# Performance work log

Hardware: AMD Instinct MI355X
Metric: run time of the kernel (lower is better)

The kernel has to match this reference:

```python
import jax, jax.numpy as jnp
import numpy as np

H = 512

def setup_inputs() -> dict:
    key = jax.random.key(0)
    k1, k2, k3, k4 = jax.random.split(key, 4)
    B, S_dec, S_enc = 8, 2048, 2048
    encoder_output = jax.random.normal(k1, (B, S_enc, H), dtype=jnp.float32)
    decoder_output = jax.random.normal(k2, (B, S_dec, H), dtype=jnp.float32)
    # nn.Bilinear(H, H, 1): weight [1, H, H], bias [1]; init U(-1/sqrt(H), 1/sqrt(H))
    bound = 1.0 / np.sqrt(H)
    W = jax.random.uniform(k3, (1, H, H), dtype=jnp.float32, minval=-bound, maxval=bound)
    b = jax.random.uniform(k4, (1,), dtype=jnp.float32, minval=-bound, maxval=bound)
    return {"encoder_output": encoder_output, "decoder_output": decoder_output, "W": W, "b": b}

def reference(encoder_output, decoder_output, W, b):
    # Original: scores[b,d,e] = Bilinear(enc[b,e], dec[b,d]) = enc[b,e] @ W[0] @ dec[b,d] + bias
    # Computed as two GEMMs instead of expanding to [B, S_dec, S_enc, H].
    encW = jnp.einsum('beh,hg->beg', encoder_output, W[0])   # [B, S_enc, H]
    scores = jnp.einsum('beg,bdg->bde', encW, decoder_output) + b[0]  # [B, S_dec, S_enc]
    return scores
```

## Files before the change

kernel.cpp:

```cpp
#include <hip/hip_runtime.h>

typedef __attribute__((ext_vector_type(8))) short short8;
typedef __attribute__((ext_vector_type(4))) float f32x4;
typedef __attribute__((ext_vector_type(8))) unsigned short ushort8;

__device__ __forceinline__ unsigned short f2bf(float x) {
  union { float f; unsigned u; } v; v.f = x;
  unsigned r = v.u + 0x7fffu + ((v.u >> 16) & 1u);
  return (unsigned short)(r >> 16);
}

__global__ __launch_bounds__(256) void wt_kernel(
    const float* __restrict__ W, unsigned short* __restrict__ Wt) {
  __shared__ float s[64][65];
  int g0 = blockIdx.x * 64, h0 = blockIdx.y * 64;
  int tx = threadIdx.x & 63, ty = threadIdx.x >> 6;
#pragma unroll
  for (int rr = 0; rr < 16; ++rr) {
    int h = ty * 16 + rr;
    s[h][tx] = W[(long)(h0 + h) * 512 + g0 + tx];
  }
  __syncthreads();
#pragma unroll
  for (int rr = 0; rr < 16; ++rr) {
    int g = ty * 16 + rr;
    Wt[(long)(g0 + g) * 512 + h0 + tx] = f2bf(s[tx][g]);
  }
}

__global__ __launch_bounds__(256) void gemm1_plus_cvtdec(
    const float* __restrict__ enc, const unsigned short* __restrict__ Wt,
    unsigned short* __restrict__ encW,
    const float* __restrict__ dec, unsigned short* __restrict__ dec_bf) {
  if (blockIdx.x >= 512) {
    int i = (blockIdx.x - 512) * 256 + threadIdx.x;
    const float4* p = (const float4*)(dec + (long)i * 8);
    float4 a = p[0], b = p[1];
    ushort8 o;
    o[0] = f2bf(a.x); o[1] = f2bf(a.y); o[2] = f2bf(a.z); o[3] = f2bf(a.w);
    o[4] = f2bf(b.x); o[5] = f2bf(b.y); o[6] = f2bf(b.z); o[7] = f2bf(b.w);
    *(ushort8*)(dec_bf + (long)i * 8) = o;
    return;
  }

  constexpr int K = 512, N = 512, BK = 32;
  __shared__ __align__(16) short As[128 * BK];
  __shared__ __align__(16) short Bs[128 * BK];

  const int g = blockIdx.x;
  const int work = (g & 7) * 64 + (g >> 3);
  const int bxm = work >> 2, byn = work & 3;

  const int tid = threadIdx.x;
  const int wave = tid >> 6, lane = tid & 63;
  const int wm = wave >> 1, wn = wave & 1;
  const int r = lane & 15, q = lane >> 4;

  const float* Ab = enc + (long)bxm * 128 * K;
  const unsigned short* Bb = Wt + (long)byn * 128 * K;

  const int srow = tid >> 1, shalf = tid & 1;
  const float* arow = Ab + (long)srow * K + shalf * 16;

  f32x4 acc[4][4] = {};
  float4 av[4];
#pragma unroll
  for (int j = 0; j < 4; ++j) av[j] = ((const float4*)arow)[j];

  for (int kt = 0; kt < K; kt += BK) {
    ushort8 o0, o1;
    o0[0] = f2bf(av[0].x); o0[1] = f2bf(av[0].y); o0[2] = f2bf(av[0].z); o0[3] = f2bf(av[0].w);
    o0[4] = f2bf(av[1].x); o0[5] = f2bf(av[1].y); o0[6] = f2bf(av[1].z); o0[7] = f2bf(av[1].w);
    o1[0] = f2bf(av[2].x); o1[1] = f2bf(av[2].y); o1[2] = f2bf(av[2].z); o1[3] = f2bf(av[2].w);
    o1[4] = f2bf(av[3].x); o1[5] = f2bf(av[3].y); o1[6] = f2bf(av[3].z); o1[7] = f2bf(av[3].w);
    *(ushort8*)&As[srow * BK + shalf * 16 + 0] = o0;
    *(ushort8*)&As[srow * BK + shalf * 16 + 8] = o1;

#pragma unroll
    for (int j = 0; j < 2; ++j) {
      int c = (j * 4 + wave) * 64 + lane;
      int row = c >> 2;
      int coff = (c & 3) * 8;
      __builtin_amdgcn_global_load_lds(
          (const __attribute__((address_space(1))) void*)(Bb + (long)row * K + kt + coff),
          (__attribute__((address_space(3))) void*)(Bs + (j * 4 + wave) * 512),
          16, 0, 0);
    }
    __syncthreads();

    short8 af[4], bfr[4];
#pragma unroll
    for (int m = 0; m < 4; ++m)
      af[m] = *(const short8*)&As[(wm * 64 + m * 16 + r) * BK + q * 8];
#pragma unroll
    for (int n = 0; n < 4; ++n)
      bfr[n] = *(const short8*)&Bs[(wn * 64 + n * 16 + r) * BK + q * 8];

    if (kt + BK < K) {
      const float* ap = arow + kt + BK;
#pragma unroll
      for (int j = 0; j < 4; ++j) av[j] = ((const float4*)ap)[j];
    }

#pragma unroll
    for (int m = 0; m < 4; ++m)
#pragma unroll
      for (int n = 0; n < 4; ++n)
        acc[m][n] = __builtin_amdgcn_mfma_f32_16x16x32_bf16(af[m], bfr[n], acc[m][n], 0, 0, 0);
    __syncthreads();
  }

  const long rowbase = (long)bxm * 128 + wm * 64;
  const long colbase = (long)byn * 128 + wn * 64;
#pragma unroll
  for (int m = 0; m < 4; ++m)
#pragma unroll
    for (int n = 0; n < 4; ++n)
#pragma unroll
      for (int j = 0; j < 4; ++j) {
        long row = rowbase + m * 16 + q * 4 + j;
        long col = colbase + n * 16 + r;
        encW[row * (long)N + col] = f2bf(acc[m][n][j]);
      }
}


#define VMCNT(n) asm volatile("s_waitcnt vmcnt(" #n ")" ::: "memory")

#define STAGE(GP, LBASE, tt, kkv)                                             \
  do {                                                                        \
    _Pragma("unroll") for (int j_ = 0; j_ < 2; ++j_) {                        \
      int c_ = w * 2 + j_;                                                    \
      __builtin_amdgcn_global_load_lds(                                       \
          (const __attribute__((address_space(1))) void*)(                    \
              (GP) + ((long)(c_ * 16 + srow)) * 512 + (tt) * 64 + (kkv) * 32 + scol), \
          (__attribute__((address_space(3))) void*)((LBASE) + (c_ << 10)),    \
          16, 0, 0);                                                          \
    }                                                                         \
  } while (0)

#define PHASE(Ac, Bc, kkv, mb, LOADB, STAGE_STMT, ENDWAIT_STMT)               \
  do {                                                                        \
    if (LOADB) {                                                              \
      _Pragma("unroll") for (int n_ = 0; n_ < 4; ++n_)                        \
        bf[kkv][n_] = *(const short8*)((Bc) + (kkv) * 16384 +                 \
                                       ((wn * 4 + n_) << 10) + lconst);       \
    }                                                                         \
    _Pragma("unroll") for (int i_ = 0; i_ < 4; ++i_)                          \
      af[i_] = *(const short8*)((Ac) + (kkv) * 16384 +                        \
                                ((wm * 8 + (mb) + i_) << 10) + lconst);       \
    STAGE_STMT;                                                               \
    __builtin_amdgcn_s_barrier();                                             \
    asm volatile("s_waitcnt lgkmcnt(0)" ::: "memory");                        \
    __builtin_amdgcn_sched_barrier(0);                                        \
    __builtin_amdgcn_s_setprio(1);                                            \
    _Pragma("unroll") for (int i_ = 0; i_ < 4; ++i_)                          \
      _Pragma("unroll") for (int n_ = 0; n_ < 4; ++n_)                        \
        acc[(mb) + i_][n_] = __builtin_amdgcn_mfma_f32_16x16x32_bf16(         \
            af[i_], bf[kkv][n_], acc[(mb) + i_][n_], 0, 0, 0);                \
    __builtin_amdgcn_s_setprio(0);                                            \
    ENDWAIT_STMT;                                                             \
    __builtin_amdgcn_s_barrier();                                             \
  } while (0)

__global__ __launch_bounds__(512, 2) void gemm2_8ph(
    const unsigned short* __restrict__ A,
    const unsigned short* __restrict__ Bt,
    float* __restrict__ C, const float* __restrict__ bias) {
  __shared__ __align__(16) char Lds[131072];
#define LDS_A(d) (Lds + (d) * 32768)
#define LDS_B(d) (Lds + 65536 + (d) * 32768)

  int flat = blockIdx.x;
  int sw = (flat & 7) * 64 + (flat >> 3);
  int z = sw >> 6, xy = sw & 63, bx = xy & 7, by = xy >> 3;

  const int tid = threadIdx.x;
  const int w = tid >> 6, lane = tid & 63;
  const int wm = w >> 2, wn = w & 3;
  const int base_r = lane & 15, q = lane >> 4;
  const int lconst = base_r * 64 + ((q * 16) ^ ((base_r & 8) << 2));
  const int srow = lane >> 2;
  const int scol = ((lane & 3) * 8) ^ (((lane >> 5) & 1) << 4);

  const unsigned short* Ab = A + ((long)z * 2048 + bx * 256) * 512;
  const unsigned short* Bb = Bt + ((long)z * 2048 + by * 256) * 512;

  f32x4 acc[8][4] = {};
  short8 af[4];
  short8 bf[2][4];

  STAGE(Ab, LDS_A(0), 0, 0);
  STAGE(Bb, LDS_B(0), 0, 0);
  STAGE(Ab, LDS_A(0) + 16384, 0, 1);
  STAGE(Bb, LDS_B(0) + 16384, 0, 1);
  VMCNT(4);
  __builtin_amdgcn_s_barrier();

  for (int t = 0; t < 7; ++t) {
    const char* Ac = LDS_A(t & 1);
    const char* Bc = LDS_B(t & 1);
    char* An = LDS_A((t + 1) & 1);
    char* Bn = LDS_B((t + 1) & 1);
    PHASE(Ac, Bc, 0, 0, true,  STAGE(Ab, An, t + 1, 0),         (void)0);
    PHASE(Ac, Bc, 0, 4, false, STAGE(Bb, Bn, t + 1, 0),         VMCNT(4));
    PHASE(Ac, Bc, 1, 0, true,  STAGE(Ab, An + 16384, t + 1, 1), (void)0);
    PHASE(Ac, Bc, 1, 4, false, STAGE(Bb, Bn + 16384, t + 1, 1), VMCNT(4));
  }
  {
    const char* Ac = LDS_A(1);
    const char* Bc = LDS_B(1);
    PHASE(Ac, Bc, 0, 0, true,  (void)0, (void)0);
    PHASE(Ac, Bc, 0, 4, false, (void)0, VMCNT(0));
    PHASE(Ac, Bc, 1, 0, true,  (void)0, (void)0);
    PHASE(Ac, Bc, 1, 4, false, (void)0, (void)0);
  }

  const float bv = bias[0];
  float* Cb = C + ((long)z * 2048 + bx * 256 + wm * 128) * 2048 + by * 256 + wn * 64;
#pragma unroll
  for (int m = 0; m < 8; ++m)
#pragma unroll
    for (int n = 0; n < 4; ++n)
#pragma unroll
      for (int j = 0; j < 4; ++j)
        Cb[(long)(m * 16 + q * 4 + j) * 2048 + n * 16 + base_r] = acc[m][n][j] + bv;
#undef LDS_A
#undef LDS_B
}

extern "C" void kernel_launch(void* const* d_in, const int* in_sizes, int n_in,
                              void* d_out, int out_size, void* d_ws, size_t ws_size,
                              hipStream_t stream) {
  const float* enc  = (const float*)d_in[0];
  const float* dec  = (const float*)d_in[1];
  const float* W    = (const float*)d_in[2];
  const float* bias = (const float*)d_in[3];
  float* out = (float*)d_out;

  constexpr int Bn = 8, S = 2048, H = 512;
  constexpr long NE = (long)Bn * S * H;

  unsigned short* dec_bf = (unsigned short*)d_ws;
  unsigned short* Wt     = dec_bf + NE;
  unsigned short* encW   = Wt + (long)H * H;

  wt_kernel<<<dim3(8, 8), 256, 0, stream>>>(W, Wt);

  gemm1_plus_cvtdec<<<dim3(512 + 4096, 1, 1), 256, 0, stream>>>(
      enc, Wt, encW, dec, dec_bf);

  gemm2_8ph<<<dim3(512, 1, 1), 512, 0, stream>>>(dec_bf, encW, out, bias);
}
```

Measured before the change: 83.47 us.

## Fuse decoder fp32-to-bf16 conversion into GEMM2 A-operand staging

Drops the separate pass that converted the decoder output to a bf16 workspace copy. GEMM2 now loads fp32 decoder rows into registers, converts them to bf16 and writes them into swizzled LDS inside its pipelined phases, while the B operand still uses direct global-to-LDS loads. This removes one write and one read of a 16 MB bf16 buffer. In exchange GEMM2 reads twice as many A bytes, each of the 8 column blocks re-reads and re-converts the fp32 A tile, and register pressure and VALU work rise in the main loop.

Result: slower. 90.09 us (+7.9%).

```diff
diff --git a/kernel.cpp b/kernel.cpp
--- a/kernel.cpp
+++ b/kernel.cpp
@@ -28,21 +28,9 @@
   }
 }
 
-__global__ __launch_bounds__(256) void gemm1_plus_cvtdec(
+__global__ __launch_bounds__(256) void gemm1_abt(
     const float* __restrict__ enc, const unsigned short* __restrict__ Wt,
-    unsigned short* __restrict__ encW,
-    const float* __restrict__ dec, unsigned short* __restrict__ dec_bf) {
-  if (blockIdx.x >= 512) {
-    int i = (blockIdx.x - 512) * 256 + threadIdx.x;
-    const float4* p = (const float4*)(dec + (long)i * 8);
-    float4 a = p[0], b = p[1];
-    ushort8 o;
-    o[0] = f2bf(a.x); o[1] = f2bf(a.y); o[2] = f2bf(a.z); o[3] = f2bf(a.w);
-    o[4] = f2bf(b.x); o[5] = f2bf(b.y); o[6] = f2bf(b.z); o[7] = f2bf(b.w);
-    *(ushort8*)(dec_bf + (long)i * 8) = o;
-    return;
-  }
-
+    unsigned short* __restrict__ encW) {
   constexpr int K = 512, N = 512, BK = 32;
   __shared__ __align__(16) short As[128 * BK];
   __shared__ __align__(16) short Bs[128 * BK];
@@ -126,32 +114,53 @@
 
 
 #define VMCNT(n) asm volatile("s_waitcnt vmcnt(" #n ")" ::: "memory")
-
-#define STAGE(GP, LBASE, tt, kkv)                                             \
+#define LGKM0 asm volatile("s_waitcnt lgkmcnt(0)" ::: "memory")
+#define BARRIER __builtin_amdgcn_s_barrier()
+
+#define BSTAGE(LBASE, tt, kkv)                                                \
   do {                                                                        \
     _Pragma("unroll") for (int j_ = 0; j_ < 2; ++j_) {                        \
       int c_ = w * 2 + j_;                                                    \
       __builtin_amdgcn_global_load_lds(                                       \
           (const __attribute__((address_space(1))) void*)(                    \
-              (GP) + ((long)(c_ * 16 + srow)) * 512 + (tt) * 64 + (kkv) * 32 + scol), \
+              Bb + ((long)(c_ * 16 + srow)) * 512 + (tt) * 64 + (kkv) * 32 + scol), \
           (__attribute__((address_space(3))) void*)((LBASE) + (c_ << 10)),    \
           16, 0, 0);                                                          \
     }                                                                         \
   } while (0)
 
-#define PHASE(Ac, Bc, kkv, mb, LOADB, STAGE_STMT, ENDWAIT_STMT)               \
-  do {                                                                        \
-    if (LOADB) {                                                              \
-      _Pragma("unroll") for (int n_ = 0; n_ < 4; ++n_)                        \
-        bf[kkv][n_] = *(const short8*)((Bc) + (kkv) * 16384 +                 \
-                                       ((wn * 4 + n_) << 10) + lconst);       \
-    }                                                                         \
-    _Pragma("unroll") for (int i_ = 0; i_ < 4; ++i_)                          \
-      af[i_] = *(const short8*)((Ac) + (kkv) * 16384 +                        \
-                                ((wm * 8 + (mb) + i_) << 10) + lconst);       \
-    STAGE_STMT;                                                               \
-    __builtin_amdgcn_s_barrier();                                             \
-    asm volatile("s_waitcnt lgkmcnt(0)" ::: "memory");                        \
+#define ALOAD(r0, r1, r2, r3, tt, kkv)                                        \
+  do {                                                                        \
+    const float* p_ = asrc + (tt) * 64 + (kkv) * 32;                          \
+    r0 = *(const float4*)(p_);                                                \
+    r1 = *(const float4*)(p_ + 4);                                            \
+    r2 = *(const float4*)(p_ + 8192);                                         \
+    r3 = *(const float4*)(p_ + 8196);                                         \
+  } while (0)
+
+#define ACVT(LBASE, kkv, r0, r1, r2, r3)                                      \
+  do {                                                                        \
+    ushort8 o0_, o1_;                                                         \
+    o0_[0] = f2bf(r0.x); o0_[1] = f2bf(r0.y); o0_[2] = f2bf(r0.z); o0_[3] = f2bf(r0.w); \
+    o0_[4] = f2bf(r1.x); o0_[5] = f2bf(r1.y); o0_[6] = f2bf(r1.z); o0_[7] = f2bf(r1.w); \
+    o1_[0] = f2bf(r2.x); o1_[1] = f2bf(r2.y); o1_[2] = f2bf(r2.z); o1_[3] = f2bf(r2.w); \
+    o1_[4] = f2bf(r3.x); o1_[5] = f2bf(r3.y); o1_[6] = f2bf(r3.z); o1_[7] = f2bf(r3.w); \
+    *(ushort8*)((LBASE) + (kkv) * 16384 + awoff) = o0_;                       \
+    *(ushort8*)((LBASE) + (kkv) * 16384 + awoff + 1024) = o1_;                \
+  } while (0)
+
+#define LOADFRAG_B(Bc, kkv)                                                   \
+  _Pragma("unroll") for (int n_ = 0; n_ < 4; ++n_)                            \
+    bf[kkv][n_] = *(const short8*)((Bc) + (kkv) * 16384 + ((wn * 4 + n_) << 10) + lconst)
+
+#define LOADFRAG_A(Ac, kkv, mb)                                               \
+  _Pragma("unroll") for (int i_ = 0; i_ < 4; ++i_)                            \
+    af[i_] = *(const short8*)((Ac) + (kkv) * 16384 + ((wm * 8 + (mb) + i_) << 10) + lconst)
+
+#define COMPUTE(kkv, mb)                                                      \
+  do {                                                                        \
+    BARRIER;                                                                  \
+    LGKM0;                                                                    \
     __builtin_amdgcn_sched_barrier(0);                                        \
     __builtin_amdgcn_s_setprio(1);                                            \
     _Pragma("unroll") for (int i_ = 0; i_ < 4; ++i_)                          \
@@ -159,12 +168,10 @@
         acc[(mb) + i_][n_] = __builtin_amdgcn_mfma_f32_16x16x32_bf16(         \
             af[i_], bf[kkv][n_], acc[(mb) + i_][n_], 0, 0, 0);                \
     __builtin_amdgcn_s_setprio(0);                                            \
-    ENDWAIT_STMT;                                                             \
-    __builtin_amdgcn_s_barrier();                                             \
   } while (0)
 
 __global__ __launch_bounds__(512, 2) void gemm2_8ph(
-    const unsigned short* __restrict__ A,
+    const float* __restrict__ dec,
     const unsigned short* __restrict__ Bt,
     float* __restrict__ C, const float* __restrict__ bias) {
   __shared__ __align__(16) char Lds[131072];
@@ -183,37 +190,78 @@
   const int srow = lane >> 2;
   const int scol = ((lane & 3) * 8) ^ (((lane >> 5) & 1) << 4);
 
-  const unsigned short* Ab = A + ((long)z * 2048 + bx * 256) * 512;
+  const float* asrc = dec + ((long)z * 2048 + bx * 256 + w * 32 + (lane >> 2)) * 512 +
+                      (((lane & 3) * 8) ^ ((lane >> 5) << 4));
+  const int awoff = w * 2048 + lane * 16;
+
   const unsigned short* Bb = Bt + ((long)z * 2048 + by * 256) * 512;
 
   f32x4 acc[8][4] = {};
   short8 af[4];
   short8 bf[2][4];
-
-  STAGE(Ab, LDS_A(0), 0, 0);
-  STAGE(Bb, LDS_B(0), 0, 0);
-  STAGE(Ab, LDS_A(0) + 16384, 0, 1);
-  STAGE(Bb, LDS_B(0) + 16384, 0, 1);
-  VMCNT(4);
-  __builtin_amdgcn_s_barrier();
+  float4 a00, a01, a02, a03;
+  float4 a10, a11, a12, a13;
+
+  ALOAD(a00, a01, a02, a03, 0, 0);
+  BSTAGE(LDS_B(0), 0, 0);
+  ALOAD(a10, a11, a12, a13, 0, 1);
+  BSTAGE(LDS_B(0) + 16384, 0, 1);
+  VMCNT(6);
+  ACVT(LDS_A(0), 0, a00, a01, a02, a03);
+  VMCNT(2);
+  ACVT(LDS_A(0), 1, a10, a11, a12, a13);
+  LGKM0;
+  BARRIER;
 
   for (int t = 0; t < 7; ++t) {
     const char* Ac = LDS_A(t & 1);
     const char* Bc = LDS_B(t & 1);
     char* An = LDS_A((t + 1) & 1);
     char* Bn = LDS_B((t + 1) & 1);
-    PHASE(Ac, Bc, 0, 0, true,  STAGE(Ab, An, t + 1, 0),         (void)0);
-    PHASE(Ac, Bc, 0, 4, false, STAGE(Bb, Bn, t + 1, 0),         VMCNT(4));
-    PHASE(Ac, Bc, 1, 0, true,  STAGE(Ab, An + 16384, t + 1, 1), (void)0);
-    PHASE(Ac, Bc, 1, 4, false, STAGE(Bb, Bn + 16384, t + 1, 1), VMCNT(4));
+    LOADFRAG_B(Bc, 0);
+    LOADFRAG_A(Ac, 0, 0);
+    ALOAD(a00, a01, a02, a03, t + 1, 0);
+    COMPUTE(0, 0);
+    BARRIER;
+    LOADFRAG_A(Ac, 0, 4);
+    BSTAGE(Bn, t + 1, 0);
+    COMPUTE(0, 4);
+    VMCNT(6);
+    BARRIER;
+    LOADFRAG_B(Bc, 1);
+    LOADFRAG_A(Ac, 1, 0);
+    ALOAD(a10, a11, a12, a13, t + 1, 1);
+    COMPUTE(1, 0);
+    VMCNT(6);
+    ACVT(An, 0, a00, a01, a02, a03);
+    LGKM0;
+    BARRIER;
+    LOADFRAG_A(Ac, 1, 4);
+    BSTAGE(Bn + 16384, t + 1, 1);
+    COMPUTE(1, 4);
+    VMCNT(2);
+    ACVT(An, 1, a10, a11, a12, a13);
+    LGKM0;
+    BARRIER;
   }
   {
     const char* Ac = LDS_A(1);
     const char* Bc = LDS_B(1);
-    PHASE(Ac, Bc, 0, 0, true,  (void)0, (void)0);
-    PHASE(Ac, Bc, 0, 4, false, (void)0, VMCNT(0));
-    PHASE(Ac, Bc, 1, 0, true,  (void)0, (void)0);
-    PHASE(Ac, Bc, 1, 4, false, (void)0, (void)0);
+    LOADFRAG_B(Bc, 0);
+    LOADFRAG_A(Ac, 0, 0);
+    COMPUTE(0, 0);
+    BARRIER;
+    LOADFRAG_A(Ac, 0, 4);
+    COMPUTE(0, 4);
+    VMCNT(0);
+    BARRIER;
+    LOADFRAG_B(Bc, 1);
+    LOADFRAG_A(Ac, 1, 0);
+    COMPUTE(1, 0);
+    BARRIER;
+    LOADFRAG_A(Ac, 1, 4);
+    COMPUTE(1, 4);
+    BARRIER;
   }
 
   const float bv = bias[0];
@@ -238,17 +286,14 @@
   const float* bias = (const float*)d_in[3];
   float* out = (float*)d_out;
 
-  constexpr int Bn = 8, S = 2048, H = 512;
-  constexpr long NE = (long)Bn * S * H;
-
-  unsigned short* dec_bf = (unsigned short*)d_ws;
-  unsigned short* Wt     = dec_bf + NE;
-  unsigned short* encW   = Wt + (long)H * H;
+  constexpr int H = 512;
+
+  unsigned short* Wt   = (unsigned short*)d_ws;
+  unsigned short* encW = Wt + (long)H * H;
 
   wt_kernel<<<dim3(8, 8), 256, 0, stream>>>(W, Wt);
 
-  gemm1_plus_cvtdec<<<dim3(512 + 4096, 1, 1), 256, 0, stream>>>(
-      enc, Wt, encW, dec, dec_bf);
-
-  gemm2_8ph<<<dim3(512, 1, 1), 512, 0, stream>>>(dec_bf, encW, out, bias);
-}
+  gemm1_abt<<<dim3(512, 1, 1), 256, 0, stream>>>(enc, Wt, encW);
+
+  gemm2_8ph<<<dim3(512, 1, 1), 512, 0, stream>>>(dec, encW, out, bias);
+}
```

## Shrink GEMM2 block tile from 256x256 to 128x128 with 256 threads

Applied to the files above, without the earlier changes.

Replaces the 512-thread 256x256 output-tile GEMM2 kernel with a 256-thread 128x128 tile kernel launched over 2048 blocks, halving LDS use per block. The phase pipeline is restructured into four half-compute steps per k-tile with the same double-buffered async global-to-LDS staging. The aim is more blocks for better CU load balance and occupancy, at the cost of lower arithmetic intensity and more global traffic per output element.

New measurement: 81.47 us. 1.02x faster.

```diff
diff --git a/kernel.cpp b/kernel.cpp
--- a/kernel.cpp
+++ b/kernel.cpp
@@ -126,100 +126,125 @@
 
 
 #define VMCNT(n) asm volatile("s_waitcnt vmcnt(" #n ")" ::: "memory")
-
-#define STAGE(GP, LBASE, tt, kkv)                                             \
+#define LGKM0 asm volatile("s_waitcnt lgkmcnt(0)" ::: "memory")
+#define BARRIER __builtin_amdgcn_s_barrier()
+
+#define STAGE2(GP, LBASE, tt, kkv)                                            \
   do {                                                                        \
     _Pragma("unroll") for (int j_ = 0; j_ < 2; ++j_) {                        \
       int c_ = w * 2 + j_;                                                    \
       __builtin_amdgcn_global_load_lds(                                       \
           (const __attribute__((address_space(1))) void*)(                    \
               (GP) + ((long)(c_ * 16 + srow)) * 512 + (tt) * 64 + (kkv) * 32 + scol), \
-          (__attribute__((address_space(3))) void*)((LBASE) + (c_ << 10)),    \
+          (__attribute__((address_space(3))) void*)((LBASE) + (kkv) * 8192 + (c_ << 10)), \
           16, 0, 0);                                                          \
     }                                                                         \
   } while (0)
 
-#define PHASE(Ac, Bc, kkv, mb, LOADB, STAGE_STMT, ENDWAIT_STMT)               \
+#define LOADFRAG_B2(Bc, kkv)                                                  \
+  _Pragma("unroll") for (int n_ = 0; n_ < 4; ++n_)                            \
+    bf[n_] = *(const short8*)((Bc) + (kkv) * 8192 + ((wn * 4 + n_) << 10) + lconst)
+
+#define LOADFRAG_A2(Ac, kkv, mh)                                              \
+  _Pragma("unroll") for (int i_ = 0; i_ < 2; ++i_)                            \
+    af[i_] = *(const short8*)((Ac) + (kkv) * 8192 + ((wm * 4 + (mh) * 2 + i_) << 10) + lconst)
+
+#define COMPUTE2(mh)                                                          \
   do {                                                                        \
-    if (LOADB) {                                                              \
-      _Pragma("unroll") for (int n_ = 0; n_ < 4; ++n_)                        \
-        bf[kkv][n_] = *(const short8*)((Bc) + (kkv) * 16384 +                 \
-                                       ((wn * 4 + n_) << 10) + lconst);       \
-    }                                                                         \
-    _Pragma("unroll") for (int i_ = 0; i_ < 4; ++i_)                          \
-      af[i_] = *(const short8*)((Ac) + (kkv) * 16384 +                        \
-                                ((wm * 8 + (mb) + i_) << 10) + lconst);       \
-    STAGE_STMT;                                                               \
-    __builtin_amdgcn_s_barrier();                                             \
-    asm volatile("s_waitcnt lgkmcnt(0)" ::: "memory");                        \
+    BARRIER;                                                                  \
+    LGKM0;                                                                    \
     __builtin_amdgcn_sched_barrier(0);                                        \
     __builtin_amdgcn_s_setprio(1);                                            \
-    _Pragma("unroll") for (int i_ = 0; i_ < 4; ++i_)                          \
+    _Pragma("unroll") for (int i_ = 0; i_ < 2; ++i_)                          \
       _Pragma("unroll") for (int n_ = 0; n_ < 4; ++n_)                        \
-        acc[(mb) + i_][n_] = __builtin_amdgcn_mfma_f32_16x16x32_bf16(         \
-            af[i_], bf[kkv][n_], acc[(mb) + i_][n_], 0, 0, 0);                \
+        acc[(mh) * 2 + i_][n_] = __builtin_amdgcn_mfma_f32_16x16x32_bf16(     \
+            af[i_], bf[n_], acc[(mh) * 2 + i_][n_], 0, 0, 0);                 \
     __builtin_amdgcn_s_setprio(0);                                            \
-    ENDWAIT_STMT;                                                             \
-    __builtin_amdgcn_s_barrier();                                             \
   } while (0)
 
-__global__ __launch_bounds__(512, 2) void gemm2_8ph(
+__global__ __launch_bounds__(256, 2) void gemm2_128(
     const unsigned short* __restrict__ A,
     const unsigned short* __restrict__ Bt,
     float* __restrict__ C, const float* __restrict__ bias) {
-  __shared__ __align__(16) char Lds[131072];
-#define LDS_A(d) (Lds + (d) * 32768)
-#define LDS_B(d) (Lds + 65536 + (d) * 32768)
+  __shared__ __align__(16) char Lds[65536];
+#define LDS_A(d) (Lds + (d) * 16384)
+#define LDS_B(d) (Lds + 32768 + (d) * 16384)
 
   int flat = blockIdx.x;
-  int sw = (flat & 7) * 64 + (flat >> 3);
-  int z = sw >> 6, xy = sw & 63, bx = xy & 7, by = xy >> 3;
+  int sw = (flat & 7) * 256 + (flat >> 3);
+  int z = sw >> 8, bx = (sw >> 4) & 15, by = sw & 15;
 
   const int tid = threadIdx.x;
   const int w = tid >> 6, lane = tid & 63;
-  const int wm = w >> 2, wn = w & 3;
+  const int wm = w >> 1, wn = w & 1;
   const int base_r = lane & 15, q = lane >> 4;
   const int lconst = base_r * 64 + ((q * 16) ^ ((base_r & 8) << 2));
   const int srow = lane >> 2;
   const int scol = ((lane & 3) * 8) ^ (((lane >> 5) & 1) << 4);
 
-  const unsigned short* Ab = A + ((long)z * 2048 + bx * 256) * 512;
-  const unsigned short* Bb = Bt + ((long)z * 2048 + by * 256) * 512;
-
-  f32x4 acc[8][4] = {};
-  short8 af[4];
-  short8 bf[2][4];
-
-  STAGE(Ab, LDS_A(0), 0, 0);
-  STAGE(Bb, LDS_B(0), 0, 0);
-  STAGE(Ab, LDS_A(0) + 16384, 0, 1);
-  STAGE(Bb, LDS_B(0) + 16384, 0, 1);
+  const unsigned short* Ab = A + ((long)z * 2048 + bx * 128) * 512;
+  const unsigned short* Bb = Bt + ((long)z * 2048 + by * 128) * 512;
+
+  f32x4 acc[4][4] = {};
+  short8 af[2];
+  short8 bf[4];
+
+  STAGE2(Ab, LDS_A(0), 0, 0);
+  STAGE2(Bb, LDS_B(0), 0, 0);
+  STAGE2(Ab, LDS_A(0), 0, 1);
+  STAGE2(Bb, LDS_B(0), 0, 1);
   VMCNT(4);
-  __builtin_amdgcn_s_barrier();
+  BARRIER;
 
   for (int t = 0; t < 7; ++t) {
     const char* Ac = LDS_A(t & 1);
     const char* Bc = LDS_B(t & 1);
     char* An = LDS_A((t + 1) & 1);
     char* Bn = LDS_B((t + 1) & 1);
-    PHASE(Ac, Bc, 0, 0, true,  STAGE(Ab, An, t + 1, 0),         (void)0);
-    PHASE(Ac, Bc, 0, 4, false, STAGE(Bb, Bn, t + 1, 0),         VMCNT(4));
-    PHASE(Ac, Bc, 1, 0, true,  STAGE(Ab, An + 16384, t + 1, 1), (void)0);
-    PHASE(Ac, Bc, 1, 4, false, STAGE(Bb, Bn + 16384, t + 1, 1), VMCNT(4));
+    LOADFRAG_B2(Bc, 0);
+    LOADFRAG_A2(Ac, 0, 0);
+    STAGE2(Ab, An, t + 1, 0);
+    COMPUTE2(0);
+    BARRIER;
+    LOADFRAG_A2(Ac, 0, 1);
+    STAGE2(Bb, Bn, t + 1, 0);
+    COMPUTE2(1);
+    VMCNT(4);
+    BARRIER;
+    LOADFRAG_B2(Bc, 1);
+    LOADFRAG_A2(Ac, 1, 0);
+    STAGE2(Ab, An, t + 1, 1);
+    COMPUTE2(0);
+    BARRIER;
+    LOADFRAG_A2(Ac, 1, 1);
+    STAGE2(Bb, Bn, t + 1, 1);
+    COMPUTE2(1);
+    VMCNT(4);
+    BARRIER;
   }
   {
     const char* Ac = LDS_A(1);
     const char* Bc = LDS_B(1);
-    PHASE(Ac, Bc, 0, 0, true,  (void)0, (void)0);
-    PHASE(Ac, Bc, 0, 4, false, (void)0, VMCNT(0));
-    PHASE(Ac, Bc, 1, 0, true,  (void)0, (void)0);
-    PHASE(Ac, Bc, 1, 4, false, (void)0, (void)0);
+    LOADFRAG_B2(Bc, 0);
+    LOADFRAG_A2(Ac, 0, 0);
+    COMPUTE2(0);
+    BARRIER;
+    LOADFRAG_A2(Ac, 0, 1);
+    COMPUTE2(1);
+    VMCNT(0);
+    BARRIER;
+    LOADFRAG_B2(Bc, 1);
+    LOADFRAG_A2(Ac, 1, 0);
+    COMPUTE2(0);
+    BARRIER;
+    LOADFRAG_A2(Ac, 1, 1);
+    COMPUTE2(1);
   }
 
   const float bv = bias[0];
-  float* Cb = C + ((long)z * 2048 + bx * 256 + wm * 128) * 2048 + by * 256 + wn * 64;
-#pragma unroll
-  for (int m = 0; m < 8; ++m)
+  float* Cb = C + ((long)z * 2048 + bx * 128 + wm * 64) * 2048 + by * 128 + wn * 64;
+#pragma unroll
+  for (int m = 0; m < 4; ++m)
 #pragma unroll
     for (int n = 0; n < 4; ++n)
 #pragma unroll
@@ -250,5 +275,5 @@
   gemm1_plus_cvtdec<<<dim3(512 + 4096, 1, 1), 256, 0, stream>>>(
       enc, Wt, encW, dec, dec_bf);
 
-  gemm2_8ph<<<dim3(512, 1, 1), 512, 0, stream>>>(dec_bf, encW, out, bias);
-}
+  gemm2_128<<<dim3(2048, 1, 1), 256, 0, stream>>>(dec_bf, encW, out, bias);
+}
```

## Make second GEMM a persistent strip kernel holding A in LDS and streaming B

Applied to the files above, without the earlier changes.

The second GEMM changes from 512 blocks of 256x256 output tiles to 256 blocks. Each block keeps a full 64x512 strip of the decoder matrix resident in LDS, then streams 8 column tiles of encW through a 4-deep buffer, writing output after each tile. This removes repeated A reloads and lets the epilogue stores overlap the next tile's loads. In exchange each block computes a smaller 64x256 tile per pass with less MFMA work per B fragment, runs at one block per CU, and the grid drops to 256 blocks.

Measured after the change: 91.37 us. 1.09x slower.

```diff
diff --git a/kernel.cpp b/kernel.cpp
--- a/kernel.cpp
+++ b/kernel.cpp
@@ -126,55 +126,64 @@
 
 
 #define VMCNT(n) asm volatile("s_waitcnt vmcnt(" #n ")" ::: "memory")
-
-#define STAGE(GP, LBASE, tt, kkv)                                             \
+#define LGKM0 asm volatile("s_waitcnt lgkmcnt(0)" ::: "memory")
+#define BARRIER __builtin_amdgcn_s_barrier()
+
+#define BSTG(LB, S2)                                                          \
   do {                                                                        \
+    int nt2_ = (S2) >> 4, ks2_ = (S2) & 15;                                   \
     _Pragma("unroll") for (int j_ = 0; j_ < 2; ++j_) {                        \
       int c_ = w * 2 + j_;                                                    \
       __builtin_amdgcn_global_load_lds(                                       \
           (const __attribute__((address_space(1))) void*)(                    \
-              (GP) + ((long)(c_ * 16 + srow)) * 512 + (tt) * 64 + (kkv) * 32 + scol), \
-          (__attribute__((address_space(3))) void*)((LBASE) + (c_ << 10)),    \
+              Bb + ((long)(nt2_ * 256 + c_ * 16 + srow)) * 512 + ks2_ * 32 + scol), \
+          (__attribute__((address_space(3))) void*)((LB) + (c_ << 10)),       \
           16, 0, 0);                                                          \
     }                                                                         \
   } while (0)
 
-#define PHASE(Ac, Bc, kkv, mb, LOADB, STAGE_STMT, ENDWAIT_STMT)               \
+#define FRAGS_MFMA(BUFI, KS)                                                  \
   do {                                                                        \
-    if (LOADB) {                                                              \
-      _Pragma("unroll") for (int n_ = 0; n_ < 4; ++n_)                        \
-        bf[kkv][n_] = *(const short8*)((Bc) + (kkv) * 16384 +                 \
-                                       ((wn * 4 + n_) << 10) + lconst);       \
+    const char* Bc_ = BLds + (BUFI) * 16384;                                  \
+    _Pragma("unroll") for (int n_ = 0; n_ < 4; ++n_)                          \
+      bf[n_] = *(const short8*)(Bc_ + ((wn * 4 + n_) << 10) + lconst);        \
+    _Pragma("unroll") for (int i_ = 0; i_ < 2; ++i_) {                        \
+      int row_ = wm * 32 + i_ * 16 + base_r;                                  \
+      af[i_] = *(const short8*)(ALds + row_ * 1024 +                          \
+                                (((KS) * 64 + q * 16) ^ ((row_ & 7) << 4)));  \
     }                                                                         \
-    _Pragma("unroll") for (int i_ = 0; i_ < 4; ++i_)                          \
-      af[i_] = *(const short8*)((Ac) + (kkv) * 16384 +                        \
-                                ((wm * 8 + (mb) + i_) << 10) + lconst);       \
-    STAGE_STMT;                                                               \
-    __builtin_amdgcn_s_barrier();                                             \
-    asm volatile("s_waitcnt lgkmcnt(0)" ::: "memory");                        \
+    LGKM0;                                                                    \
     __builtin_amdgcn_sched_barrier(0);                                        \
     __builtin_amdgcn_s_setprio(1);                                            \
-    _Pragma("unroll") for (int i_ = 0; i_ < 4; ++i_)                          \
+    _Pragma("unroll") for (int i_ = 0; i_ < 2; ++i_)                          \
       _Pragma("unroll") for (int n_ = 0; n_ < 4; ++n_)                        \
-        acc[(mb) + i_][n_] = __builtin_amdgcn_mfma_f32_16x16x32_bf16(         \
-            af[i_], bf[kkv][n_], acc[(mb) + i_][n_], 0, 0, 0);                \
+        acc[i_][n_] = __builtin_amdgcn_mfma_f32_16x16x32_bf16(                \
+            af[i_], bf[n_], acc[i_][n_], 0, 0, 0);                            \
     __builtin_amdgcn_s_setprio(0);                                            \
-    ENDWAIT_STMT;                                                             \
-    __builtin_amdgcn_s_barrier();                                             \
   } while (0)
 
-__global__ __launch_bounds__(512, 2) void gemm2_8ph(
+#define EPILOGUE(NT)                                                          \
+  do {                                                                        \
+    float* Cb_ = C + ((long)z * 2048 + strip * 64 + wm * 32) * 2048 +         \
+                 (NT) * 256 + wn * 64;                                        \
+    _Pragma("unroll") for (int m_ = 0; m_ < 2; ++m_)                          \
+      _Pragma("unroll") for (int n_ = 0; n_ < 4; ++n_)                        \
+        _Pragma("unroll") for (int j_ = 0; j_ < 4; ++j_)                      \
+          Cb_[(long)(m_ * 16 + q * 4 + j_) * 2048 + n_ * 16 + base_r] =       \
+              acc[m_][n_][j_] + bv;                                           \
+    _Pragma("unroll") for (int m_ = 0; m_ < 2; ++m_)                          \
+      _Pragma("unroll") for (int n_ = 0; n_ < 4; ++n_)                        \
+        acc[m_][n_] = (f32x4){0.f, 0.f, 0.f, 0.f};                            \
+  } while (0)
+
+__global__ __launch_bounds__(512, 1) void gemm2_persist(
     const unsigned short* __restrict__ A,
     const unsigned short* __restrict__ Bt,
     float* __restrict__ C, const float* __restrict__ bias) {
   __shared__ __align__(16) char Lds[131072];
-#define LDS_A(d) (Lds + (d) * 32768)
-#define LDS_B(d) (Lds + 65536 + (d) * 32768)
-
-  int flat = blockIdx.x;
-  int sw = (flat & 7) * 64 + (flat >> 3);
-  int z = sw >> 6, xy = sw & 63, bx = xy & 7, by = xy >> 3;
-
+
+  const int blk = blockIdx.x;
+  const int z = blk & 7, strip = blk >> 3;
   const int tid = threadIdx.x;
   const int w = tid >> 6, lane = tid & 63;
   const int wm = w >> 2, wn = w & 3;
@@ -183,50 +192,72 @@
   const int srow = lane >> 2;
   const int scol = ((lane & 3) * 8) ^ (((lane >> 5) & 1) << 4);
 
-  const unsigned short* Ab = A + ((long)z * 2048 + bx * 256) * 512;
-  const unsigned short* Bb = Bt + ((long)z * 2048 + by * 256) * 512;
-
-  f32x4 acc[8][4] = {};
-  short8 af[4];
-  short8 bf[2][4];
-
-  STAGE(Ab, LDS_A(0), 0, 0);
-  STAGE(Bb, LDS_B(0), 0, 0);
-  STAGE(Ab, LDS_A(0) + 16384, 0, 1);
-  STAGE(Bb, LDS_B(0) + 16384, 0, 1);
+  const unsigned short* Arow0 = A + ((long)z * 2048 + strip * 64) * 512;
+  const unsigned short* Bb = Bt + (long)z * 2048 * 512;
+  char* ALds = Lds;
+  char* BLds = Lds + 65536;
+
+  f32x4 acc[2][4] = {};
+  short8 af[2];
+  short8 bf[4];
+
+  ushort8 areg[8];
+  const int arw = tid >> 6, acolb = (tid & 63) * 16;
+#pragma unroll
+  for (int i = 0; i < 8; ++i)
+    areg[i] = *(const ushort8*)((const char*)Arow0 + (long)(i * 8 + arw) * 1024 + acolb);
+  BSTG(BLds + 0 * 16384, 0);
+  BSTG(BLds + 1 * 16384, 1);
   VMCNT(4);
-  __builtin_amdgcn_s_barrier();
-
-  for (int t = 0; t < 7; ++t) {
-    const char* Ac = LDS_A(t & 1);
-    const char* Bc = LDS_B(t & 1);
-    char* An = LDS_A((t + 1) & 1);
-    char* Bn = LDS_B((t + 1) & 1);
-    PHASE(Ac, Bc, 0, 0, true,  STAGE(Ab, An, t + 1, 0),         (void)0);
-    PHASE(Ac, Bc, 0, 4, false, STAGE(Bb, Bn, t + 1, 0),         VMCNT(4));
-    PHASE(Ac, Bc, 1, 0, true,  STAGE(Ab, An + 16384, t + 1, 1), (void)0);
-    PHASE(Ac, Bc, 1, 4, false, STAGE(Bb, Bn + 16384, t + 1, 1), VMCNT(4));
-  }
-  {
-    const char* Ac = LDS_A(1);
-    const char* Bc = LDS_B(1);
-    PHASE(Ac, Bc, 0, 0, true,  (void)0, (void)0);
-    PHASE(Ac, Bc, 0, 4, false, (void)0, VMCNT(0));
-    PHASE(Ac, Bc, 1, 0, true,  (void)0, (void)0);
-    PHASE(Ac, Bc, 1, 4, false, (void)0, (void)0);
-  }
+#pragma unroll
+  for (int i = 0; i < 8; ++i) {
+    int row = i * 8 + arw;
+    *(ushort8*)(ALds + row * 1024 + (acolb ^ ((row & 7) << 4))) = areg[i];
+  }
+  LGKM0;
 
   const float bv = bias[0];
-  float* Cb = C + ((long)z * 2048 + bx * 256 + wm * 128) * 2048 + by * 256 + wn * 64;
-#pragma unroll
-  for (int m = 0; m < 8; ++m)
-#pragma unroll
-    for (int n = 0; n < 4; ++n)
-#pragma unroll
-      for (int j = 0; j < 4; ++j)
-        Cb[(long)(m * 16 + q * 4 + j) * 2048 + n * 16 + base_r] = acc[m][n][j] + bv;
-#undef LDS_A
-#undef LDS_B
+
+  for (int nt = 0; nt < 8; ++nt) {
+    const int s0 = nt * 16;
+    BSTG(BLds + ((s0 + 2) & 3) * 16384, s0 + 2);
+    VMCNT(4);
+    BARRIER;
+    if (nt > 0) EPILOGUE(nt - 1);
+    FRAGS_MFMA(s0 & 3, 0);
+    BSTG(BLds + ((s0 + 3) & 3) * 16384, s0 + 3);
+    if (nt == 0) { VMCNT(4); } else { VMCNT(36); }
+    BARRIER;
+    FRAGS_MFMA((s0 + 1) & 3, 1);
+    BSTG(BLds + ((s0 + 4) & 3) * 16384, s0 + 4);
+    if (nt == 0) { VMCNT(4); } else { VMCNT(36); }
+    BARRIER;
+    FRAGS_MFMA((s0 + 2) & 3, 2);
+    for (int ks = 3; ks <= 13; ++ks) {
+      const int s = s0 + ks;
+      BSTG(BLds + ((s + 2) & 3) * 16384, s + 2);
+      VMCNT(4);
+      BARRIER;
+      FRAGS_MFMA(s & 3, ks);
+    }
+    if (nt < 7) {
+      BSTG(BLds + ((s0 + 16) & 3) * 16384, s0 + 16);
+      VMCNT(4);
+    } else {
+      VMCNT(2);
+    }
+    BARRIER;
+    FRAGS_MFMA((s0 + 14) & 3, 14);
+    if (nt < 7) {
+      BSTG(BLds + ((s0 + 17) & 3) * 16384, s0 + 17);
+      VMCNT(4);
+    } else {
+      VMCNT(0);
+    }
+    BARRIER;
+    FRAGS_MFMA((s0 + 15) & 3, 15);
+  }
+  EPILOGUE(7);
 }
 
 extern "C" void kernel_launch(void* const* d_in, const int* in_sizes, int n_in,
@@ -250,5 +281,5 @@
   gemm1_plus_cvtdec<<<dim3(512 + 4096, 1, 1), 256, 0, stream>>>(
       enc, Wt, encW, dec, dec_bf);
 
-  gemm2_8ph<<<dim3(512, 1, 1), 512, 0, stream>>>(dec_bf, encW, out, bias);
-}
+  gemm2_persist<<<dim3(256, 1, 1), 512, 0, stream>>>(dec_bf, encW, out, bias);
+}
```
